# Kernel optimization log

Hardware: AMD Instinct MI355X
Metric: run time of the kernel (lower is better)

Reference implementation:

```python
import jax, jax.numpy as jnp
import numpy as np

IN_DIM = 1024
QK_DIM = 64
NHEADS = 12
HN_MULT = 4
BATCH = 2
SEQ = 2048
BETA = 1.0 / np.sqrt(QK_DIM)


def setup_inputs() -> dict:
    key = jax.random.key(0)
    kg, kq, kk, kw = jax.random.split(key, 4)
    scale = 1.0 / np.sqrt(IN_DIM)
    g = jax.random.normal(kg, (BATCH, SEQ, IN_DIM), dtype=jnp.float32)
    Wq = jax.random.normal(kq, (NHEADS, QK_DIM, IN_DIM), dtype=jnp.float32) * scale
    Wk = jax.random.normal(kk, (NHEADS, QK_DIM, IN_DIM), dtype=jnp.float32) * scale
    Whn = jax.random.normal(kw, (HN_MULT * IN_DIM, IN_DIM), dtype=jnp.float32) * scale
    return {"g": g, "Wq": Wq, "Wk": Wk, "Whn": Whn}


def reference(g, Wq, Wk, Whn):
    # --- attention energy (Energy Transformer): E = -(1/beta) * sum logsumexp_keys(beta * q.k)
    q = jnp.einsum("bnd,hkd->bhnk", g, Wq)  # [B,H,N,K]
    k = jnp.einsum("bnd,hkd->bhnk", g, Wk)  # [B,H,N,K]
    scores = BETA * jnp.einsum("bhnk,bhmk->bhnm", q, k)  # [B,H,N(query),M(key)]
    e_attn = -(1.0 / BETA) * jnp.sum(jax.nn.logsumexp(scores, axis=-1))
    # --- Hopfield energy: -0.5 * sum(relu(W g)^2)
    h = jnp.einsum("bnd,md->bnm", g, Whn)  # [B,N,4*D]
    e_hn = -0.5 * jnp.sum(jax.nn.relu(h) ** 2)
    return e_attn + e_hn
```

## Files before the change

kernel.cpp:

```cpp
#include <hip/hip_runtime.h>
#include <hip/hip_bf16.h>

typedef __attribute__((ext_vector_type(4))) float f32x4;
typedef __attribute__((ext_vector_type(8))) short bf16x8;
typedef unsigned short u16;
typedef __attribute__((ext_vector_type(4))) u16 u16x4;


#define OFF_GB    ((size_t)0)
#define OFF_WQB   ((size_t)8388608)
#define OFF_WKB   ((size_t)(8388608+1572864))
#define OFF_WHNB  ((size_t)(8388608+2*1572864))
#define OFF_QB    (OFF_WHNB + 8388608)
#define OFF_KB    (OFF_QB + 6291456)

__device__ __forceinline__ u16 f2bf(float f) {
  union { float f; unsigned u; } x; x.f = f;
  unsigned u = x.u;
  u += 0x7fffu + ((u >> 16) & 1u);
  return (u16)(u >> 16);
}

__global__ __launch_bounds__(256) void convert_all(
    const float* __restrict__ g, const float* __restrict__ wq,
    const float* __restrict__ wk, const float* __restrict__ whn,
    u16* __restrict__ gB, u16* __restrict__ wqB, u16* __restrict__ wkB, u16* __restrict__ whnB)
{
  const int NG = 1048576;
  const int NW = 196608;
  const int total = NG + 2 * NW + NG;
  for (int i = blockIdx.x * blockDim.x + threadIdx.x; i < total; i += gridDim.x * blockDim.x) {
    const float4* src; u16* dst; int j; float scale = 1.0f;
    if (i < NG)              { src = (const float4*)g;   dst = gB;   j = i; }
    else if (i < NG + NW)    { src = (const float4*)wq;  dst = wqB;  j = i - NG;
                               scale = 0.125f * 1.44269504089f; }
    else if (i < NG + 2*NW)  { src = (const float4*)wk;  dst = wkB;  j = i - NG - NW; }
    else                     { src = (const float4*)whn; dst = whnB; j = i - NG - 2*NW; }
    float4 v = src[j];
    u16x4 o;
    o.x = f2bf(v.x * scale); o.y = f2bf(v.y * scale);
    o.z = f2bf(v.z * scale); o.w = f2bf(v.w * scale);
    *(u16x4*)(dst + (size_t)j * 4) = o;
  }
}

__global__ __launch_bounds__(256) void gemm_bt(
    const u16* __restrict__ A, const u16* __restrict__ B0, const u16* __restrict__ B1,
    u16* __restrict__ C0, u16* __restrict__ C1, int K)
{
  __shared__ u16 lA[128 * 64];
  __shared__ u16 lB[128 * 64];
  const int tid = threadIdx.x;
  const int lane = tid & 63;
  const int w = tid >> 6;
  const int bid = blockIdx.x;
  const int xcd = bid & 7, idx = bid >> 3;
  const int bm = ((xcd >> 1) << 3) + (idx & 7);
  const int bn = (xcd & 1) * 6 + (idx >> 3);

  const u16* Bp; u16* Cp; int bcol0;
  if (bn < 6) { Bp = B0; Cp = C0; bcol0 = bn * 128; }
  else        { Bp = B1; Cp = C1; bcol0 = (bn - 6) * 128; }
  const int arow0 = bm * 128;
  const int wr = w >> 1, wc = w & 1;
  const int l15 = lane & 15, lg = lane >> 4;

  f32x4 acc[4][4];
  const f32x4 zz = {0.f, 0.f, 0.f, 0.f};
#pragma unroll
  for (int m = 0; m < 4; m++)
#pragma unroll
    for (int n = 0; n < 4; n++) acc[m][n] = zz;

#define STAGE(KT) do {                                                                     \
    _Pragma("unroll")                                                                      \
    for (int i = 0; i < 4; i++) {                                                          \
      int rloc = w * 32 + i * 8 + (lane >> 3);                                             \
      int cb   = (((lane & 7) ^ (rloc & 7)) << 4);                                         \
      const char* srcA = (const char*)A + (((size_t)(arow0 + rloc)) * K + (KT) * 64) * 2 + cb; \
      __builtin_amdgcn_global_load_lds((const __attribute__((address_space(1))) void*)srcA, \
          (__attribute__((address_space(3))) void*)((char*)lA + (w * 32 + i * 8) * 128), 16, 0, 0); \
      const char* srcB = (const char*)Bp + (((size_t)(bcol0 + rloc)) * K + (KT) * 64) * 2 + cb; \
      __builtin_amdgcn_global_load_lds((const __attribute__((address_space(1))) void*)srcB, \
          (__attribute__((address_space(3))) void*)((char*)lB + (w * 32 + i * 8) * 128), 16, 0, 0); \
    }                                                                                      \
  } while (0)

  STAGE(0);
  const int nkt = K / 64;
  for (int kt = 0; kt < nkt; ++kt) {
    __syncthreads();
    bf16x8 a0[4], a1[4], b0[4], b1[4];
#pragma unroll
    for (int m = 0; m < 4; m++) {
      int row = wr * 64 + m * 16 + l15;
      const char* base = (const char*)lA + row * 128;
      int sw = (row & 7) << 4;
      a0[m] = *(const bf16x8*)(base + ((lg * 16) ^ sw));
      a1[m] = *(const bf16x8*)(base + ((64 + lg * 16) ^ sw));
    }
#pragma unroll
    for (int n = 0; n < 4; n++) {
      int row = wc * 64 + n * 16 + l15;
      const char* base = (const char*)lB + row * 128;
      int sw = (row & 7) << 4;
      b0[n] = *(const bf16x8*)(base + ((lg * 16) ^ sw));
      b1[n] = *(const bf16x8*)(base + ((64 + lg * 16) ^ sw));
    }
    __syncthreads();
    if (kt + 1 < nkt) STAGE(kt + 1);
#pragma unroll
    for (int m = 0; m < 4; m++)
#pragma unroll
      for (int n = 0; n < 4; n++) {
        acc[m][n] = __builtin_amdgcn_mfma_f32_16x16x32_bf16(a0[m], b0[n], acc[m][n], 0, 0, 0);
        acc[m][n] = __builtin_amdgcn_mfma_f32_16x16x32_bf16(a1[m], b1[n], acc[m][n], 0, 0, 0);
      }
  }
#pragma unroll
  for (int m = 0; m < 4; m++)
#pragma unroll
    for (int n = 0; n < 4; n++)
#pragma unroll
      for (int r = 0; r < 4; r++) {
        int row = arow0 + wr * 64 + m * 16 + lg * 4 + r;
        int col = bcol0 + wc * 64 + n * 16 + l15;
        size_t dst = ((((size_t)(row >> 11) * 12 + (col >> 6)) << 11) + (row & 2047)) * 64 + (col & 63);
        Cp[dst] = f2bf(acc[m][n][r]);
      }
#undef STAGE
}

__global__ __launch_bounds__(512, 4) void hop_gemm(
    const u16* __restrict__ A, const u16* __restrict__ Bm, float* __restrict__ out)
{
  __shared__ __align__(16) u16 lds[3][(256 + 128) * 32];
  const int tid = threadIdx.x;
  const int lane = tid & 63, w = tid >> 6;
  const int wr = w >> 1, wc = w & 1;
  const int l15 = lane & 15, lg = lane >> 4;
  const int bid = blockIdx.x;
  const int xcd = bid & 7, idx = bid >> 3;
  const int am0 = (((xcd >> 1) << 2) + (idx & 3)) * 256;
  const int bn0 = (((xcd & 1) << 4) + (idx >> 2)) * 128;
  constexpr int nkt = 32;

  f32x4 acc[4][4];
  const f32x4 zz = {0.f, 0.f, 0.f, 0.f};
#pragma unroll
  for (int m = 0; m < 4; m++)
#pragma unroll
    for (int n = 0; n < 4; n++) acc[m][n] = zz;

#define HSTAGE(KT) do {                                                                    \
    char* s0_ = (char*)&lds[(KT) % 3][0];                                                  \
    _Pragma("unroll")                                                                      \
    for (int i_ = 0; i_ < 2; i_++) {                                                       \
      int r_ = i_ * 128 + (tid >> 2);                                                      \
      int cb_ = ((tid & 3) * 16) ^ ((r_ & 3) << 4);                                        \
      const char* g_ = (const char*)A + (size_t)(am0 + r_) * 2048 + (KT) * 64 + cb_;       \
      __builtin_amdgcn_global_load_lds((const __attribute__((address_space(1))) void*)g_,  \
          (__attribute__((address_space(3))) void*)(s0_ + i_ * 8192 + tid * 16), 16, 0, 0);\
    }                                                                                      \
    {                                                                                      \
      int r_ = tid >> 2;                                                                   \
      int cb_ = ((tid & 3) * 16) ^ ((r_ & 3) << 4);                                        \
      const char* g_ = (const char*)Bm + (size_t)(bn0 + r_) * 2048 + (KT) * 64 + cb_;      \
      __builtin_amdgcn_global_load_lds((const __attribute__((address_space(1))) void*)g_,  \
          (__attribute__((address_space(3))) void*)(s0_ + 16384 + tid * 16), 16, 0, 0);    \
    }                                                                                      \
  } while (0)

#define LDA2(DST, SL, M) do {                                                              \
    int r_ = wr * 64 + (M) * 16 + l15;                                                     \
    DST = *(const bf16x8*)((const char*)&lds[(SL)][0] + r_ * 64 + ((lg * 16) ^ ((r_ & 3) << 4))); \
  } while (0)
#define LDB2(DST, SL, N) do {                                                              \
    int r_ = wc * 64 + (N) * 16 + l15;                                                     \
    DST = *(const bf16x8*)((const char*)&lds[(SL)][0] + 16384 + r_ * 64 + ((lg * 16) ^ ((r_ & 3) << 4))); \
  } while (0)

  HSTAGE(0);
  HSTAGE(1);
  asm volatile("s_waitcnt vmcnt(3)" ::: "memory");
  __builtin_amdgcn_s_barrier();

  for (int t = 0; t < nkt; ++t) {
    const int sl = t % 3;
    if (t + 2 < nkt) HSTAGE(t + 2);
    bf16x8 av[4], bv[4];
#pragma unroll
    for (int m = 0; m < 4; m++) LDA2(av[m], sl, m);
#pragma unroll
    for (int n = 0; n < 4; n++) LDB2(bv[n], sl, n);
    __builtin_amdgcn_s_setprio(1);
#pragma unroll
    for (int m = 0; m < 4; m++)
#pragma unroll
      for (int n = 0; n < 4; n++)
        acc[m][n] = __builtin_amdgcn_mfma_f32_16x16x32_bf16(av[m], bv[n], acc[m][n], 0, 0, 0);
    __builtin_amdgcn_s_setprio(0);
    if (t + 2 < nkt)      asm volatile("s_waitcnt vmcnt(3)" ::: "memory");
    else if (t + 1 < nkt) asm volatile("s_waitcnt vmcnt(0)" ::: "memory");
    if (t + 1 < nkt) __builtin_amdgcn_s_barrier();
  }
#undef HSTAGE
#undef LDA2
#undef LDB2

  float loc = 0.f;
#pragma unroll
  for (int m = 0; m < 4; m++)
#pragma unroll
    for (int n = 0; n < 4; n++)
#pragma unroll
      for (int r = 0; r < 4; r++) {
        float v = acc[m][n][r];
        loc += (v > 0.f) ? v * v : 0.f;
      }
#pragma unroll
  for (int mask = 32; mask; mask >>= 1) loc += __shfl_xor(loc, mask, 64);
  if (lane == 0) atomicAdd(out, -0.5f * loc);
}

__global__ __launch_bounds__(256) void scores_lse(
    const u16* __restrict__ qB, const u16* __restrict__ kB, float* __restrict__ out)
{
  __shared__ __align__(16) u16 kbuf[3][128 * 64];
  const int z  = blockIdx.x;
  const int qt = blockIdx.y;
  const int tid = threadIdx.x, lane = tid & 63, w = tid >> 6;
  const int l15 = lane & 15, lg = lane >> 4;

  const u16* qp = qB + ((size_t)z * 2048 + qt * 64 + w * 16 + l15) * 64 + lg * 8;
  bf16x8 qf0 = *(const bf16x8*)qp;
  bf16x8 qf1 = *(const bf16x8*)(qp + 32);

#define KSTAGE(KB, BUF) do {                                                               \
    _Pragma("unroll")                                                                      \
    for (int i = 0; i < 4; i++) {                                                          \
      int rloc = i * 32 + w * 8 + (lane >> 3);                                             \
      int cb   = (((lane & 7) ^ (rloc & 7)) << 4);                                         \
      const char* src = (const char*)kB + ((size_t)z * 2048 + (KB) * 128 + rloc) * 128 + cb; \
      __builtin_amdgcn_global_load_lds((const __attribute__((address_space(1))) void*)src,  \
          (__attribute__((address_space(3))) void*)((char*)kbuf[(BUF)] + rloc * 128 + (lane & 7) * 16), 16, 0, 0); \
    }                                                                                      \
  } while (0)

  f32x4 sacc = {0.f, 0.f, 0.f, 0.f};
  const f32x4 zz = {0.f, 0.f, 0.f, 0.f};

  KSTAGE(0, 0);
  KSTAGE(1, 1);
  asm volatile("s_waitcnt vmcnt(4)" ::: "memory");
  __builtin_amdgcn_s_barrier();
  __builtin_amdgcn_sched_barrier(0);

  const int NKB = 16;
  for (int kb = 0; kb < NKB; ++kb) {
    if (kb + 2 < NKB) KSTAGE(kb + 2, (kb + 2) % 3);
    const char* cur = (const char*)kbuf[kb % 3];
#pragma unroll
    for (int g2 = 0; g2 < 8; ++g2) {
      int row = g2 * 16 + l15;
      const char* base = cur + row * 128;
      int sw = (row & 7) << 4;
      bf16x8 b0 = *(const bf16x8*)(base + ((lg * 16) ^ sw));
      bf16x8 b1 = *(const bf16x8*)(base + ((64 + lg * 16) ^ sw));
      f32x4 s = zz;
      s = __builtin_amdgcn_mfma_f32_16x16x32_bf16(qf0, b0, s, 0, 0, 0);
      s = __builtin_amdgcn_mfma_f32_16x16x32_bf16(qf1, b1, s, 0, 0, 0);
      sacc[0] += __builtin_amdgcn_exp2f(s[0]);
      sacc[1] += __builtin_amdgcn_exp2f(s[1]);
      sacc[2] += __builtin_amdgcn_exp2f(s[2]);
      sacc[3] += __builtin_amdgcn_exp2f(s[3]);
    }
    if (kb + 1 < NKB) {
      if (kb + 2 < NKB) asm volatile("s_waitcnt vmcnt(4)" ::: "memory");
      else              asm volatile("s_waitcnt vmcnt(0)" ::: "memory");
      __builtin_amdgcn_s_barrier();
      __builtin_amdgcn_sched_barrier(0);
    }
  }
#undef KSTAGE

#pragma unroll
  for (int mask = 8; mask; mask >>= 1) {
    sacc[0] += __shfl_xor(sacc[0], mask, 64);
    sacc[1] += __shfl_xor(sacc[1], mask, 64);
    sacc[2] += __shfl_xor(sacc[2], mask, 64);
    sacc[3] += __shfl_xor(sacc[3], mask, 64);
  }
  float part = 0.f;
  if (l15 == 0) {
    part = __builtin_amdgcn_logf(sacc[0]) + __builtin_amdgcn_logf(sacc[1]) +
           __builtin_amdgcn_logf(sacc[2]) + __builtin_amdgcn_logf(sacc[3]);
  }
  part += __shfl_xor(part, 16, 64);
  part += __shfl_xor(part, 32, 64);
  if (lane == 0) atomicAdd(out, -5.5451774444795625f * part);
}

extern "C" void kernel_launch(void* const* d_in, const int* in_sizes, int n_in,
                              void* d_out, int out_size, void* d_ws, size_t ws_size,
                              hipStream_t stream)
{
  const float* g   = (const float*)d_in[0];
  const float* Wq  = (const float*)d_in[1];
  const float* Wk  = (const float*)d_in[2];
  const float* Whn = (const float*)d_in[3];
  float* out = (float*)d_out;
  char* ws = (char*)d_ws;

  u16* gB   = (u16*)(ws + OFF_GB);
  u16* wqB  = (u16*)(ws + OFF_WQB);
  u16* wkB  = (u16*)(ws + OFF_WKB);
  u16* whnB = (u16*)(ws + OFF_WHNB);
  u16* qB   = (u16*)(ws + OFF_QB);
  u16* kB   = (u16*)(ws + OFF_KB);

  (void)hipMemsetAsync(out, 0, sizeof(float), stream);

  convert_all<<<2048, 256, 0, stream>>>(g, Wq, Wk, Whn, gB, wqB, wkB, whnB);
  gemm_bt<<<384, 256, 0, stream>>>(gB, wqB, wkB, qB, kB, 1024);
  hop_gemm<<<512, 512, 0, stream>>>(gB, whnB, out);
  scores_lse<<<dim3(24, 32), 256, 0, stream>>>(qB, kB, out);
}
```

Measured before the change: 230.0 us.

## Rewrite hop_gemm as single-buffer 128x128 tile with 64-wide K steps

Replaces the 256x128 tile, 512-thread, triple-buffered Hopfield GEMM with a 128x128 tile, 256-thread kernel. It uses a single LDS buffer and 64-element K steps, reading fragments into registers before issuing the next global-to-LDS load. This halves LDS use, doubles the block count and uses fewer barriers per K, meant to raise occupancy and simplify the pipeline. The cost is less overlap between loads and MFMA, since the next stage's load is only issued after the current tile has been read into registers.

```diff
diff --git a/kernel.cpp b/kernel.cpp
--- a/kernel.cpp
+++ b/kernel.cpp
@@ -131,19 +131,23 @@
 #undef STAGE
 }
 
-__global__ __launch_bounds__(512, 4) void hop_gemm(
+__global__ __launch_bounds__(256) void hop_gemm(
     const u16* __restrict__ A, const u16* __restrict__ Bm, float* __restrict__ out)
 {
-  __shared__ __align__(16) u16 lds[3][(256 + 128) * 32];
+  __shared__ u16 lA[128 * 64];
+  __shared__ u16 lB[128 * 64];
   const int tid = threadIdx.x;
-  const int lane = tid & 63, w = tid >> 6;
+  const int lane = tid & 63;
+  const int w = tid >> 6;
+  const int bid = blockIdx.x;
+  const int xcd = bid & 7, idx = bid >> 3;
+  const int bm = ((xcd >> 1) << 3) + (idx & 7);
+  const int bn = ((xcd & 1) << 4) + (idx >> 3);
+  const int arow0 = bm * 128;
+  const int bcol0 = bn * 128;
   const int wr = w >> 1, wc = w & 1;
   const int l15 = lane & 15, lg = lane >> 4;
-  const int bid = blockIdx.x;
-  const int xcd = bid & 7, idx = bid >> 3;
-  const int am0 = (((xcd >> 1) << 2) + (idx & 3)) * 256;
-  const int bn0 = (((xcd & 1) << 4) + (idx >> 2)) * 128;
-  constexpr int nkt = 32;
+  constexpr int K = 1024;
 
   f32x4 acc[4][4];
   const f32x4 zz = {0.f, 0.f, 0.f, 0.f};
@@ -153,60 +157,51 @@
     for (int n = 0; n < 4; n++) acc[m][n] = zz;
 
 #define HSTAGE(KT) do {                                                                    \
-    char* s0_ = (char*)&lds[(KT) % 3][0];                                                  \
     _Pragma("unroll")                                                                      \
-    for (int i_ = 0; i_ < 2; i_++) {                                                       \
-      int r_ = i_ * 128 + (tid >> 2);                                                      \
-      int cb_ = ((tid & 3) * 16) ^ ((r_ & 3) << 4);                                        \
-      const char* g_ = (const char*)A + (size_t)(am0 + r_) * 2048 + (KT) * 64 + cb_;       \
-      __builtin_amdgcn_global_load_lds((const __attribute__((address_space(1))) void*)g_,  \
-          (__attribute__((address_space(3))) void*)(s0_ + i_ * 8192 + tid * 16), 16, 0, 0);\
-    }                                                                                      \
-    {                                                                                      \
-      int r_ = tid >> 2;                                                                   \
-      int cb_ = ((tid & 3) * 16) ^ ((r_ & 3) << 4);                                        \
-      const char* g_ = (const char*)Bm + (size_t)(bn0 + r_) * 2048 + (KT) * 64 + cb_;      \
-      __builtin_amdgcn_global_load_lds((const __attribute__((address_space(1))) void*)g_,  \
-          (__attribute__((address_space(3))) void*)(s0_ + 16384 + tid * 16), 16, 0, 0);    \
+    for (int i = 0; i < 4; i++) {                                                          \
+      int rloc = w * 32 + i * 8 + (lane >> 3);                                             \
+      int cb   = (((lane & 7) ^ (rloc & 7)) << 4);                                         \
+      const char* srcA = (const char*)A + (((size_t)(arow0 + rloc)) * K + (KT) * 64) * 2 + cb; \
+      __builtin_amdgcn_global_load_lds((const __attribute__((address_space(1))) void*)srcA, \
+          (__attribute__((address_space(3))) void*)((char*)lA + (w * 32 + i * 8) * 128), 16, 0, 0); \
+      const char* srcB = (const char*)Bm + (((size_t)(bcol0 + rloc)) * K + (KT) * 64) * 2 + cb; \
+      __builtin_amdgcn_global_load_lds((const __attribute__((address_space(1))) void*)srcB, \
+          (__attribute__((address_space(3))) void*)((char*)lB + (w * 32 + i * 8) * 128), 16, 0, 0); \
     }                                                                                      \
   } while (0)
 
-#define LDA2(DST, SL, M) do {                                                              \
-    int r_ = wr * 64 + (M) * 16 + l15;                                                     \
-    DST = *(const bf16x8*)((const char*)&lds[(SL)][0] + r_ * 64 + ((lg * 16) ^ ((r_ & 3) << 4))); \
-  } while (0)
-#define LDB2(DST, SL, N) do {                                                              \
-    int r_ = wc * 64 + (N) * 16 + l15;                                                     \
-    DST = *(const bf16x8*)((const char*)&lds[(SL)][0] + 16384 + r_ * 64 + ((lg * 16) ^ ((r_ & 3) << 4))); \
-  } while (0)
-
   HSTAGE(0);
-  HSTAGE(1);
-  asm volatile("s_waitcnt vmcnt(3)" ::: "memory");
-  __builtin_amdgcn_s_barrier();
-
-  for (int t = 0; t < nkt; ++t) {
-    const int sl = t % 3;
-    if (t + 2 < nkt) HSTAGE(t + 2);
-    bf16x8 av[4], bv[4];
-#pragma unroll
-    for (int m = 0; m < 4; m++) LDA2(av[m], sl, m);
-#pragma unroll
-    for (int n = 0; n < 4; n++) LDB2(bv[n], sl, n);
-    __builtin_amdgcn_s_setprio(1);
+  const int nkt = K / 64;
+  for (int kt = 0; kt < nkt; ++kt) {
+    __syncthreads();
+    bf16x8 a0[4], a1[4], b0[4], b1[4];
+#pragma unroll
+    for (int m = 0; m < 4; m++) {
+      int row = wr * 64 + m * 16 + l15;
+      const char* base = (const char*)lA + row * 128;
+      int sw = (row & 7) << 4;
+      a0[m] = *(const bf16x8*)(base + ((lg * 16) ^ sw));
+      a1[m] = *(const bf16x8*)(base + ((64 + lg * 16) ^ sw));
+    }
+#pragma unroll
+    for (int n = 0; n < 4; n++) {
+      int row = wc * 64 + n * 16 + l15;
+      const char* base = (const char*)lB + row * 128;
+      int sw = (row & 7) << 4;
+      b0[n] = *(const bf16x8*)(base + ((lg * 16) ^ sw));
+      b1[n] = *(const bf16x8*)(base + ((64 + lg * 16) ^ sw));
+    }
+    __syncthreads();
+    if (kt + 1 < nkt) HSTAGE(kt + 1);
 #pragma unroll
     for (int m = 0; m < 4; m++)
 #pragma unroll
-      for (int n = 0; n < 4; n++)
-        acc[m][n] = __builtin_amdgcn_mfma_f32_16x16x32_bf16(av[m], bv[n], acc[m][n], 0, 0, 0);
-    __builtin_amdgcn_s_setprio(0);
-    if (t + 2 < nkt)      asm volatile("s_waitcnt vmcnt(3)" ::: "memory");
-    else if (t + 1 < nkt) asm volatile("s_waitcnt vmcnt(0)" ::: "memory");
-    if (t + 1 < nkt) __builtin_amdgcn_s_barrier();
+      for (int n = 0; n < 4; n++) {
+        acc[m][n] = __builtin_amdgcn_mfma_f32_16x16x32_bf16(a0[m], b0[n], acc[m][n], 0, 0, 0);
+        acc[m][n] = __builtin_amdgcn_mfma_f32_16x16x32_bf16(a1[m], b1[n], acc[m][n], 0, 0, 0);
+      }
   }
 #undef HSTAGE
-#undef LDA2
-#undef LDB2
 
   float loc = 0.f;
 #pragma unroll
@@ -323,6 +318,6 @@
 
   convert_all<<<2048, 256, 0, stream>>>(g, Wq, Wk, Whn, gB, wqB, wkB, whnB);
   gemm_bt<<<384, 256, 0, stream>>>(gB, wqB, wkB, qB, kB, 1024);
-  hop_gemm<<<512, 512, 0, stream>>>(gB, whnB, out);
+  hop_gemm<<<1024, 256, 0, stream>>>(gB, whnB, out);
   scores_lse<<<dim3(24, 32), 256, 0, stream>>>(qB, kB, out);
 }
```

After: 231.5 us. About the same (+0.7%).
